# Kernel tuning notes

Measured on AMD Instinct MI355X. Metric: run time of the kernel, lower is better.

The kernel has to match this reference:

```python
import jax, jax.numpy as jnp
import numpy as np

T_STEPS = 64   # number of actions (T-1 in the torch code)
BATCH = 512
STATE = 256
ACTION = 64
BELIEF = 1024
HIDDEN = 1024
EMB = 1024
MIN_STD = 0.1


def setup_inputs() -> dict:
    key = jax.random.key(0)
    ks = jax.random.split(key, 16)
    def w(k, shape):
        return jax.random.normal(k, shape, jnp.float32) * 0.02
    return {
        "s_0": jax.random.normal(ks[0], (BATCH, STATE), jnp.float32),
        "A": jax.random.normal(ks[1], (T_STEPS, BATCH, ACTION), jnp.float32),
        "b_0": jax.random.normal(ks[2], (BATCH, BELIEF), jnp.float32),
        "O": jax.random.normal(ks[3], (T_STEPS, BATCH, EMB), jnp.float32),
        "M": jnp.ones((T_STEPS, BATCH, 1), jnp.float32),
        "noise_pri": jax.random.normal(ks[4], (T_STEPS, BATCH, STATE), jnp.float32),
        "noise_pos": jax.random.normal(ks[5], (T_STEPS, BATCH, STATE), jnp.float32),
        # learned parameters (torch nn.Linear convention: y = x @ W.T + b)
        "W_sa": w(ks[6], (BELIEF, STATE + ACTION)), "b_sa": jnp.zeros((BELIEF,), jnp.float32),
        "W_ih": w(ks[7], (3 * BELIEF, BELIEF)), "b_ih": jnp.zeros((3 * BELIEF,), jnp.float32),
        "W_hh": w(ks[8], (3 * BELIEF, BELIEF)), "b_hh": jnp.zeros((3 * BELIEF,), jnp.float32),
        "W_bpri": w(ks[9], (HIDDEN, BELIEF)), "b_bpri": jnp.zeros((HIDDEN,), jnp.float32),
        "W_spri": w(ks[10], (2 * STATE, HIDDEN)), "b_spri": jnp.zeros((2 * STATE,), jnp.float32),
        "W_bpos": w(ks[11], (HIDDEN, BELIEF + EMB)), "b_bpos": jnp.zeros((HIDDEN,), jnp.float32),
        "W_spos": w(ks[12], (2 * STATE, HIDDEN)), "b_spos": jnp.zeros((2 * STATE,), jnp.float32),
    }


def reference(s_0, A, b_0, O, M, noise_pri, noise_pos,
              W_sa, b_sa, W_ih, b_ih, W_hh, b_hh,
              W_bpri, b_bpri, W_spri, b_spri,
              W_bpos, b_bpos, W_spos, b_spos):
    act = jax.nn.relu  # cfg.activation_function = 'relu'

    def gru_cell(x, h):
        # torch GRUCell gate order: r, z, n
        gi = x @ W_ih.T + b_ih      # [B, 3*BELIEF]
        gh = h @ W_hh.T + b_hh
        i_r, i_z, i_n = jnp.split(gi, 3, axis=1)
        h_r, h_z, h_n = jnp.split(gh, 3, axis=1)
        r = jax.nn.sigmoid(i_r + h_r)
        z = jax.nn.sigmoid(i_z + h_z)
        n = jnp.tanh(i_n + r * h_n)
        return (1.0 - z) * n + z * h

    def step(carry, xs):
        b, s = carry  # belief [B,BELIEF], posterior state [B,STATE]
        a_t, o_t, m_t, eps_p, eps_q = xs
        s_in = s * m_t  # non-terminal mask
        x = act(jnp.concatenate([s_in, a_t], axis=1) @ W_sa.T + b_sa)
        b_new = gru_cell(x, b)
        # prior
        pri = act(b_new @ W_bpri.T + b_bpri) @ W_spri.T + b_spri
        mu_p, hp = jnp.split(pri, 2, axis=1)
        std_p = jax.nn.softplus(hp) + MIN_STD
        s_p = mu_p + std_p * eps_p
        # posterior (uses current observation embedding)
        pos = act(jnp.concatenate([b_new, o_t], axis=1) @ W_bpos.T + b_bpos) @ W_spos.T + b_spos
        mu_q, hq = jnp.split(pos, 2, axis=1)
        std_q = jax.nn.softplus(hq) + MIN_STD
        s_q = mu_q + std_q * eps_q
        return (b_new, s_q), (b_new, s_p, mu_p, std_p, s_q, mu_q, std_q)

    (_, _), ys = jax.lax.scan(step, (b_0, s_0), (A, O, M, noise_pri, noise_pos))
    B_out, S_pri, MU_pri, STD_pri, S_pos, MU_pos, STD_pos = ys
    return B_out, S_pri, MU_pri, STD_pri, S_pos, MU_pos, STD_pos
```

## Files before the change

### kernel.cpp

```cpp
#include <hip/hip_runtime.h>
#include <hip/hip_bf16.h>
#include <math.h>

typedef short bf16x8 __attribute__((ext_vector_type(8)));
typedef float f32x4 __attribute__((ext_vector_type(4)));
typedef unsigned short u16;

#define NT 64
#define NB 512
#define NS 256
#define NA 64
#define NBEL 1024

#define OUT_B      0
#define OUT_SPRI   33554432
#define OUT_MUPRI  41943040
#define OUT_STDPRI 50331648
#define OUT_SPOS   58720256
#define OUT_MUPOS  67108864
#define OUT_STDPOS 75497472

__device__ __forceinline__ f32x4 mfma16(bf16x8 a, bf16x8 b, f32x4 c) {
  return __builtin_amdgcn_mfma_f32_16x16x32_bf16(a, b, c, 0, 0, 0);
}

__device__ __forceinline__ u16 f2bf(float f) {
  union { float f; unsigned u; } v; v.f = f;
  return (u16)((v.u + 0x7FFFu + ((v.u >> 16) & 1u)) >> 16);
}

__device__ __forceinline__ bf16x8 ld8bf(const u16* p) { return *(const bf16x8*)p; }

__device__ __forceinline__ bf16x8 cvt8(const float* p) {
  const float4 lo = *(const float4*)p;
  const float4 hi = *(const float4*)(p + 4);
  bf16x8 v;
  v[0] = (short)f2bf(lo.x); v[1] = (short)f2bf(lo.y);
  v[2] = (short)f2bf(lo.z); v[3] = (short)f2bf(lo.w);
  v[4] = (short)f2bf(hi.x); v[5] = (short)f2bf(hi.y);
  v[6] = (short)f2bf(hi.z); v[7] = (short)f2bf(hi.w);
  return v;
}

__device__ __forceinline__ float sigm(float x) { return 1.f / (1.f + __expf(-x)); }
__device__ __forceinline__ float softplus_(float x) {
  if (x > 20.f) return x;
  return log1pf(__expf(x));
}

#define ZACC(acc) { acc[0][0] = (f32x4){0.f,0.f,0.f,0.f}; acc[0][1] = (f32x4){0.f,0.f,0.f,0.f}; \
                    acc[1][0] = (f32x4){0.f,0.f,0.f,0.f}; acc[1][1] = (f32x4){0.f,0.f,0.f,0.f}; }

#define Q4(acc, a0v, a1v, b0v, b1v) \
  acc[0][0] = mfma16(a0v, b0v, acc[0][0]); \
  acc[0][1] = mfma16(a0v, b1v, acc[0][1]); \
  acc[1][0] = mfma16(a1v, b0v, acc[1][0]); \
  acc[1][1] = mfma16(a1v, b1v, acc[1][1]);

__device__ __forceinline__ void red_write(float* L, f32x4 (&acc)[2][2], int l) {
  const int base = l * 16;
#pragma unroll
  for (int i = 0; i < 2; ++i)
#pragma unroll
    for (int j = 0; j < 2; ++j)
#pragma unroll
      for (int q = 0; q < 4; ++q)
        L[base + (i * 2 + j) * 4 + q] = acc[i][j][q];
}
__device__ __forceinline__ void red_add(const float* L, f32x4 (&acc)[2][2], int l) {
  const int base = l * 16;
#pragma unroll
  for (int i = 0; i < 2; ++i)
#pragma unroll
    for (int j = 0; j < 2; ++j)
#pragma unroll
      for (int q = 0; q < 4; ++q)
        acc[i][j][q] += L[base + (i * 2 + j) * 4 + q];
}

__device__ __forceinline__ void setflag_blk(unsigned* f) {
  __syncthreads();
  if (threadIdx.x == 0)
    __hip_atomic_fetch_add(f, 1u, __ATOMIC_RELEASE, __HIP_MEMORY_SCOPE_AGENT);
}
__device__ __forceinline__ void waitflag_blk(unsigned* f, unsigned target) {
  if (threadIdx.x == 0) {
    while (__hip_atomic_load(f, __ATOMIC_RELAXED, __HIP_MEMORY_SCOPE_AGENT) < target)
      __builtin_amdgcn_s_sleep(2);
    (void)__hip_atomic_load(f, __ATOMIC_ACQUIRE, __HIP_MEMORY_SCOPE_AGENT);
  }
  __syncthreads();
}

__global__ __launch_bounds__(256) void cvt_weights_k(
    const float* __restrict__ wsa, const float* __restrict__ wih,
    const float* __restrict__ whh, const float* __restrict__ wbpri,
    const float* __restrict__ wspri, const float* __restrict__ wbpos,
    const float* __restrict__ wspos, u16* __restrict__ dst) {
  const int S0 = 327680;
  const int S1 = S0 + 3145728;
  const int S2 = S1 + 3145728;
  const int S3 = S2 + 1048576;
  const int S4 = S3 + 524288;
  const int S5 = S4 + 2097152;
  const int S6 = S5 + 524288;
  for (int i = blockIdx.x * blockDim.x + threadIdx.x; i < S6;
       i += gridDim.x * blockDim.x) {
    float v;
    if (i < S0) v = wsa[i];
    else if (i < S1) v = wih[i - S0];
    else if (i < S2) v = whh[i - S1];
    else if (i < S3) v = wbpri[i - S2];
    else if (i < S4) v = wspri[i - S3];
    else if (i < S5) v = wbpos[i - S4];
    else v = wspos[i - S5];
    dst[i] = f2bf(v);
  }
}

__global__ __launch_bounds__(256) void init_carry_k(
    const float* __restrict__ s0, const float* __restrict__ b0,
    const float* __restrict__ Mptr, u16* __restrict__ smask,
    u16* __restrict__ bbf0, float* __restrict__ hf,
    unsigned* __restrict__ flags) {
  for (int i = blockIdx.x * blockDim.x + threadIdx.x; i < NB * NBEL;
       i += gridDim.x * blockDim.x) {
    float b = b0[i];
    bbf0[i] = f2bf(b);
    hf[i] = b;
    if (i < NB * NS) {
      int row = i >> 8;
      smask[i] = f2bf(s0[i] * Mptr[row]);
    }
    if (i < NT) flags[i] = 0;
  }
}

__device__ __forceinline__ void dev_spri(
    int g, int wid, int kh, int r16, int kq, int l, int tt,
    const u16* __restrict__ hpri, const u16* __restrict__ wspri,
    const float* __restrict__ bspri, const float* __restrict__ npri,
    float* __restrict__ out, float* lred0, float* lred1) {
  const int bm = g >> 2, bn = g & 3;
  const int row0 = bm * 64 + (wid >> 1) * 32;
  const int c0 = bn * 64 + (wid & 1) * 32;
  f32x4 am[2][2], ah[2][2];
  ZACC(am); ZACC(ah);
  const u16* A0 = hpri + (row0 + r16) * NBEL + kh * 512 + kq * 8;
  const u16* A1 = A0 + 16 * NBEL;
  const u16* Bm0 = wspri + (size_t)(c0 + r16) * NBEL + kh * 512 + kq * 8;
  const u16* Bm1 = Bm0 + 16 * NBEL;
  const u16* Bh0 = wspri + (size_t)(c0 + 256 + r16) * NBEL + kh * 512 + kq * 8;
  const u16* Bh1 = Bh0 + 16 * NBEL;
#pragma unroll 4
  for (int k = 0; k < 512; k += 32) {
    bf16x8 a0 = ld8bf(A0 + k), a1 = ld8bf(A1 + k);
    bf16x8 m0 = ld8bf(Bm0 + k), m1 = ld8bf(Bm1 + k);
    Q4(am, a0, a1, m0, m1);
    bf16x8 h0 = ld8bf(Bh0 + k), h1 = ld8bf(Bh1 + k);
    Q4(ah, a0, a1, h0, h1);
  }
  if (kh == 1) {
    red_write(lred0, am, l);
    red_write(lred1, ah, l);
  }
  __syncthreads();
  if (kh == 0) {
    red_add(lred0, am, l);
    red_add(lred1, ah, l);
#pragma unroll
    for (int i = 0; i < 2; ++i)
#pragma unroll
      for (int j = 0; j < 2; ++j)
#pragma unroll
        for (int q = 0; q < 4; ++q) {
          const int row = row0 + i * 16 + kq * 4 + q;
          const int c = c0 + j * 16 + r16;
          const size_t idx = (size_t)tt * (NB * NS) + (size_t)row * NS + c;
          const float mu = am[i][j][q] + bspri[c];
          const float hp = ah[i][j][q] + bspri[c + 256];
          const float sd = softplus_(hp) + 0.1f;
          out[OUT_SPRI + idx] = mu + sd * npri[idx];
          out[OUT_MUPRI + idx] = mu;
          out[OUT_STDPRI + idx] = sd;
        }
  }
}

__device__ __forceinline__ void dev_x(
    int g, int wid, int kh, int r16, int kq, int l, int t,
    const u16* __restrict__ smask, const float* __restrict__ Af,
    const u16* __restrict__ wsa, const float* __restrict__ bsa,
    u16* __restrict__ xg, float* lred) {
  const int bm = g >> 4, bn = g & 15;
  const int row0 = bm * 64 + (wid >> 1) * 32;
  const int col0 = bn * 64 + (wid & 1) * 32;
  f32x4 acc[2][2]; ZACC(acc);
  const u16* A0 = smask + (row0 + r16) * NS + kq * 8;
  const u16* A1 = A0 + 16 * NS;
  const u16* B0 = wsa + (size_t)(col0 + r16) * 320 + kq * 8;
  const u16* B1 = B0 + 16 * 320;
  if (kh == 0) {
#pragma unroll
    for (int k = 0; k < 160; k += 32) {
      bf16x8 a0 = ld8bf(A0 + k), a1 = ld8bf(A1 + k);
      bf16x8 b0 = ld8bf(B0 + k), b1 = ld8bf(B1 + k);
      Q4(acc, a0, a1, b0, b1);
    }
  } else {
#pragma unroll
    for (int k = 160; k < 256; k += 32) {
      bf16x8 a0 = ld8bf(A0 + k), a1 = ld8bf(A1 + k);
      bf16x8 b0 = ld8bf(B0 + k), b1 = ld8bf(B1 + k);
      Q4(acc, a0, a1, b0, b1);
    }
    const float* F0 = Af + (size_t)t * (NB * NA) + (size_t)(row0 + r16) * NA + kq * 8;
    const float* F1 = F0 + 16 * NA;
    const u16* C0 = wsa + (size_t)(col0 + r16) * 320 + 256 + kq * 8;
    const u16* C1 = C0 + 16 * 320;
#pragma unroll
    for (int k = 0; k < 64; k += 32) {
      bf16x8 a0 = cvt8(F0 + k), a1 = cvt8(F1 + k);
      bf16x8 b0 = ld8bf(C0 + k), b1 = ld8bf(C1 + k);
      Q4(acc, a0, a1, b0, b1);
    }
    red_write(lred, acc, l);
  }
  __syncthreads();
  if (kh == 0) {
    red_add(lred, acc, l);
#pragma unroll
    for (int i = 0; i < 2; ++i)
#pragma unroll
      for (int j = 0; j < 2; ++j)
#pragma unroll
        for (int q = 0; q < 4; ++q) {
          const int row = row0 + i * 16 + kq * 4 + q;
          const int col = col0 + j * 16 + r16;
          xg[row * NBEL + col] = f2bf(fmaxf(acc[i][j][q] + bsa[col], 0.f));
        }
  }
}

__global__ __launch_bounds__(512, 2) void kX0(
    const u16* __restrict__ smask, const float* __restrict__ Af,
    const u16* __restrict__ wsa, const float* __restrict__ bsa,
    u16* __restrict__ xg, const float* __restrict__ Of,
    const u16* __restrict__ wbpos, float* __restrict__ hbO0) {
  __shared__ float lred[4][1024];
  const int l = threadIdx.x & 63, r16 = l & 15, kq = l >> 4;
  const int wid8 = threadIdx.x >> 6;
  const int wid = wid8 & 3, kh = wid8 >> 2;
  if (blockIdx.x < 128) {
    dev_x(blockIdx.x, wid, kh, r16, kq, l, 0, smask, Af, wsa, bsa, xg,
          lred[wid]);
  } else {
    const int g = blockIdx.x - 128, bm = g >> 4, bn = g & 15;
    const int row0 = bm * 64 + (wid >> 1) * 32;
    const int col0 = bn * 64 + (wid & 1) * 32;
    f32x4 acc[2][2]; ZACC(acc);
    const float* F0 = Of + (row0 + r16) * NBEL + kh * 512 + kq * 8;
    const float* F1 = F0 + 16 * NBEL;
    const u16* B0 = wbpos + (size_t)(col0 + r16) * 2048 + 1024 + kh * 512 + kq * 8;
    const u16* B1 = B0 + 16 * 2048;
#pragma unroll 4
    for (int k = 0; k < 512; k += 32) {
      bf16x8 a0 = cvt8(F0 + k), a1 = cvt8(F1 + k);
      bf16x8 b0 = ld8bf(B0 + k), b1 = ld8bf(B1 + k);
      Q4(acc, a0, a1, b0, b1);
    }
    if (kh == 1) red_write(lred[wid], acc, l);
    __syncthreads();
    if (kh == 0) {
      red_add(lred[wid], acc, l);
#pragma unroll
      for (int i = 0; i < 2; ++i)
#pragma unroll
        for (int j = 0; j < 2; ++j)
#pragma unroll
          for (int q = 0; q < 4; ++q) {
            const int row = row0 + i * 16 + kq * 4 + q;
            const int col = col0 + j * 16 + r16;
            hbO0[row * NBEL + col] = acc[i][j][q];
          }
    }
  }
}

__global__ __launch_bounds__(512, 2) void kL1(
    const u16* __restrict__ xg, const u16* __restrict__ bprev,
    const u16* __restrict__ wih, const u16* __restrict__ whh,
    const float* __restrict__ bih, const float* __restrict__ bhh,
    float* __restrict__ hf, u16* __restrict__ bcur, float* __restrict__ out,
    const u16* __restrict__ hpri, const u16* __restrict__ wspri,
    const float* __restrict__ bspri, const float* __restrict__ npri, int t) {
  __shared__ float lred[4][3][1024];
  const int l = threadIdx.x & 63, r16 = l & 15, kq = l >> 4;
  const int wid8 = threadIdx.x >> 6;
  const int wid = wid8 & 3, kh = wid8 >> 2;
  if (blockIdx.x < 128) {
    const int g = blockIdx.x, bm = g >> 4, bn = g & 15;
    const int row0 = bm * 64 + (wid >> 1) * 32;
    const int col0 = bn * 64 + (wid & 1) * 32;
    f32x4 ar[2][2], az[2][2], an[2][2];
    ZACC(ar); ZACC(az); ZACC(an);
    const u16* Asrc = (kh == 0) ? xg : bprev;
    const u16* W = (kh == 0) ? wih : whh;
    const u16* A0 = Asrc + (row0 + r16) * NBEL + kq * 8;
    const u16* A1 = A0 + 16 * NBEL;
    const u16* Br0 = W + (size_t)(col0 + r16) * NBEL + kq * 8;
    const u16* Br1 = Br0 + 16 * NBEL;
    const u16* Bz0 = W + (size_t)(col0 + 1024 + r16) * NBEL + kq * 8;
    const u16* Bz1 = Bz0 + 16 * NBEL;
    const u16* Bn0 = W + (size_t)(col0 + 2048 + r16) * NBEL + kq * 8;
    const u16* Bn1 = Bn0 + 16 * NBEL;
#pragma unroll 4
    for (int k = 0; k < NBEL; k += 32) {
      bf16x8 a0 = ld8bf(A0 + k), a1 = ld8bf(A1 + k);
      bf16x8 b0 = ld8bf(Br0 + k), b1 = ld8bf(Br1 + k);
      Q4(ar, a0, a1, b0, b1);
      bf16x8 c0 = ld8bf(Bz0 + k), c1 = ld8bf(Bz1 + k);
      Q4(az, a0, a1, c0, c1);
      bf16x8 d0 = ld8bf(Bn0 + k), d1 = ld8bf(Bn1 + k);
      Q4(an, a0, a1, d0, d1);
    }
    if (kh == 1) {
      red_write(&lred[wid][0][0], ar, l);
      red_write(&lred[wid][1][0], az, l);
      red_write(&lred[wid][2][0], an, l);
    }
    __syncthreads();
    if (kh == 0) {
      const int base = l * 16;
#pragma unroll
      for (int i = 0; i < 2; ++i)
#pragma unroll
        for (int j = 0; j < 2; ++j)
#pragma unroll
          for (int q = 0; q < 4; ++q) {
            const int row = row0 + i * 16 + kq * 4 + q;
            const int c = col0 + j * 16 + r16;
            const int li = base + (i * 2 + j) * 4 + q;
            const float r = sigm(ar[i][j][q] + bih[c] + lred[wid][0][li] + bhh[c]);
            const float z = sigm(az[i][j][q] + bih[c + 1024] + lred[wid][1][li] + bhh[c + 1024]);
            const float n = tanhf(an[i][j][q] + bih[c + 2048] +
                                  r * (lred[wid][2][li] + bhh[c + 2048]));
            const float h = hf[row * NBEL + c];
            const float bnew = (1.f - z) * n + z * h;
            hf[row * NBEL + c] = bnew;
            bcur[row * NBEL + c] = f2bf(bnew);
            out[OUT_B + (size_t)t * (NB * NBEL) + row * NBEL + c] = bnew;
          }
    }
  } else if (t >= 1) {
    dev_spri(blockIdx.x - 128, wid, kh, r16, kq, l, t - 1,
             hpri, wspri, bspri, npri, out,
             &lred[wid][0][0], &lred[wid][1][0]);
  }
}

__global__ __launch_bounds__(512, 2) void kL2(
    const u16* __restrict__ bcur, const u16* __restrict__ wbpos,
    const float* __restrict__ bbpos, const float* __restrict__ hbOc,
    u16* __restrict__ hbbf,
    const u16* __restrict__ wbpri, const float* __restrict__ bbpri,
    u16* __restrict__ hpri,
    const float* __restrict__ Of, float* __restrict__ hbOn, int t) {
  __shared__ float lred[4][1024];
  const int l = threadIdx.x & 63, r16 = l & 15, kq = l >> 4;
  const int wid8 = threadIdx.x >> 6;
  const int wid = wid8 & 3, kh = wid8 >> 2;
  if (blockIdx.x < 128) {
    const int g = blockIdx.x, bm = g >> 4, bn = g & 15;
    const int row0 = bm * 64 + (wid >> 1) * 32;
    const int col0 = bn * 64 + (wid & 1) * 32;
    f32x4 acc[2][2]; ZACC(acc);
    const u16* A0 = bcur + (row0 + r16) * NBEL + kh * 512 + kq * 8;
    const u16* A1 = A0 + 16 * NBEL;
    const u16* B0 = wbpos + (size_t)(col0 + r16) * 2048 + kh * 512 + kq * 8;
    const u16* B1 = B0 + 16 * 2048;
#pragma unroll 4
    for (int k = 0; k < 512; k += 32) {
      bf16x8 a0 = ld8bf(A0 + k), a1 = ld8bf(A1 + k);
      bf16x8 b0 = ld8bf(B0 + k), b1 = ld8bf(B1 + k);
      Q4(acc, a0, a1, b0, b1);
    }
    if (kh == 1) red_write(lred[wid], acc, l);
    __syncthreads();
    if (kh == 0) {
      red_add(lred[wid], acc, l);
#pragma unroll
      for (int i = 0; i < 2; ++i)
#pragma unroll
        for (int j = 0; j < 2; ++j)
#pragma unroll
          for (int q = 0; q < 4; ++q) {
            const int row = row0 + i * 16 + kq * 4 + q;
            const int col = col0 + j * 16 + r16;
            const float v = acc[i][j][q] + hbOc[row * NBEL + col] + bbpos[col];
            hbbf[row * NBEL + col] = f2bf(fmaxf(v, 0.f));
          }
    }
  } else if (blockIdx.x < 256) {
    const int g = blockIdx.x - 128, bm = g >> 4, bn = g & 15;
    const int row0 = bm * 64 + (wid >> 1) * 32;
    const int col0 = bn * 64 + (wid & 1) * 32;
    f32x4 acc[2][2]; ZACC(acc);
    const u16* A0 = bcur + (row0 + r16) * NBEL + kh * 512 + kq * 8;
    const u16* A1 = A0 + 16 * NBEL;
    const u16* B0 = wbpri + (size_t)(col0 + r16) * NBEL + kh * 512 + kq * 8;
    const u16* B1 = B0 + 16 * NBEL;
#pragma unroll 4
    for (int k = 0; k < 512; k += 32) {
      bf16x8 a0 = ld8bf(A0 + k), a1 = ld8bf(A1 + k);
      bf16x8 b0 = ld8bf(B0 + k), b1 = ld8bf(B1 + k);
      Q4(acc, a0, a1, b0, b1);
    }
    if (kh == 1) red_write(lred[wid], acc, l);
    __syncthreads();
    if (kh == 0) {
      red_add(lred[wid], acc, l);
#pragma unroll
      for (int i = 0; i < 2; ++i)
#pragma unroll
        for (int j = 0; j < 2; ++j)
#pragma unroll
          for (int q = 0; q < 4; ++q) {
            const int row = row0 + i * 16 + kq * 4 + q;
            const int col = col0 + j * 16 + r16;
            hpri[row * NBEL + col] = f2bf(fmaxf(acc[i][j][q] + bbpri[col], 0.f));
          }
    }
  } else {
    if (t + 1 >= NT) return;
    const int g = blockIdx.x - 256, bm = g >> 4, bn = g & 15;
    const int row0 = bm * 64 + (wid >> 1) * 32;
    const int col0 = bn * 64 + (wid & 1) * 32;
    f32x4 acc[2][2]; ZACC(acc);
    const float* F0 = Of + (size_t)(t + 1) * (NB * NBEL) + (row0 + r16) * NBEL + kh * 512 + kq * 8;
    const float* F1 = F0 + 16 * NBEL;
    const u16* B0 = wbpos + (size_t)(col0 + r16) * 2048 + 1024 + kh * 512 + kq * 8;
    const u16* B1 = B0 + 16 * 2048;
#pragma unroll 4
    for (int k = 0; k < 512; k += 32) {
      bf16x8 a0 = cvt8(F0 + k), a1 = cvt8(F1 + k);
      bf16x8 b0 = ld8bf(B0 + k), b1 = ld8bf(B1 + k);
      Q4(acc, a0, a1, b0, b1);
    }
    if (kh == 1) red_write(lred[wid], acc, l);
    __syncthreads();
    if (kh == 0) {
      red_add(lred[wid], acc, l);
#pragma unroll
      for (int i = 0; i < 2; ++i)
#pragma unroll
        for (int j = 0; j < 2; ++j)
#pragma unroll
          for (int q = 0; q < 4; ++q) {
            const int row = row0 + i * 16 + kq * 4 + q;
            const int col = col0 + j * 16 + r16;
            hbOn[row * NBEL + col] = acc[i][j][q];
          }
    }
  }
}

__global__ __launch_bounds__(512, 2) void kLX(
    const u16* __restrict__ hbbf, const u16* __restrict__ wspos,
    const float* __restrict__ bspos, const float* __restrict__ npos,
    const float* __restrict__ Mptr, float* __restrict__ out,
    u16* __restrict__ smask,
    const float* __restrict__ Af, const u16* __restrict__ wsa,
    const float* __restrict__ bsa, u16* __restrict__ xg,
    const u16* __restrict__ hpri, const u16* __restrict__ wspri,
    const float* __restrict__ bspri, const float* __restrict__ npri,
    unsigned* __restrict__ flags, int t) {
  __shared__ float lred[4][2][1024];
  const int l = threadIdx.x & 63, r16 = l & 15, kq = l >> 4;
  const int wid8 = threadIdx.x >> 6;
  const int wid = wid8 & 3, kh = wid8 >> 2;
  if (blockIdx.x < 32) {
    const int g = blockIdx.x, bm = g >> 2, bn = g & 3;
    const int row0 = bm * 64 + (wid >> 1) * 32;
    const int c0 = bn * 64 + (wid & 1) * 32;
    f32x4 am[2][2], ah[2][2];
    ZACC(am); ZACC(ah);
    const u16* A0 = hbbf + (row0 + r16) * NBEL + kh * 512 + kq * 8;
    const u16* A1 = A0 + 16 * NBEL;
    const u16* Bm0 = wspos + (size_t)(c0 + r16) * NBEL + kh * 512 + kq * 8;
    const u16* Bm1 = Bm0 + 16 * NBEL;
    const u16* Bh0 = wspos + (size_t)(c0 + 256 + r16) * NBEL + kh * 512 + kq * 8;
    const u16* Bh1 = Bh0 + 16 * NBEL;
#pragma unroll 4
    for (int k = 0; k < 512; k += 32) {
      bf16x8 a0 = ld8bf(A0 + k), a1 = ld8bf(A1 + k);
      bf16x8 m0 = ld8bf(Bm0 + k), m1 = ld8bf(Bm1 + k);
      Q4(am, a0, a1, m0, m1);
      bf16x8 h0 = ld8bf(Bh0 + k), h1 = ld8bf(Bh1 + k);
      Q4(ah, a0, a1, h0, h1);
    }
    if (kh == 1) {
      red_write(&lred[wid][0][0], am, l);
      red_write(&lred[wid][1][0], ah, l);
    }
    __syncthreads();
    if (kh == 0) {
      red_add(&lred[wid][0][0], am, l);
      red_add(&lred[wid][1][0], ah, l);
#pragma unroll
      for (int i = 0; i < 2; ++i)
#pragma unroll
        for (int j = 0; j < 2; ++j)
#pragma unroll
          for (int q = 0; q < 4; ++q) {
            const int row = row0 + i * 16 + kq * 4 + q;
            const int c = c0 + j * 16 + r16;
            const float mu = am[i][j][q] + bspos[c];
            const float hq = ah[i][j][q] + bspos[c + 256];
            const float sd = softplus_(hq) + 0.1f;
            const size_t idx = (size_t)t * (NB * NS) + (size_t)row * NS + c;
            const float sq = mu + sd * npos[idx];
            out[OUT_SPOS + idx] = sq;
            out[OUT_MUPOS + idx] = mu;
            out[OUT_STDPOS + idx] = sd;
            const float mn = (t < NT - 1) ? Mptr[(t + 1) * NB + row] : 1.f;
            smask[row * NS + c] = f2bf(sq * mn);
          }
    }
    setflag_blk(&flags[t]);
  } else if (blockIdx.x < 160) {
    if (t + 1 >= NT) return;
    waitflag_blk(&flags[t], 32);
    dev_x(blockIdx.x - 32, wid, kh, r16, kq, l, t + 1, smask, Af, wsa, bsa,
          xg, &lred[wid][0][0]);
  } else {
    if (t == NT - 1)
      dev_spri(blockIdx.x - 160, wid, kh, r16, kq, l, t,
               hpri, wspri, bspri, npri, out,
               &lred[wid][0][0], &lred[wid][1][0]);
  }
}

extern "C" void kernel_launch(void* const* d_in, const int* in_sizes, int n_in,
                              void* d_out, int out_size, void* d_ws, size_t ws_size,
                              hipStream_t stream) {
  const float* s0 = (const float*)d_in[0];
  const float* Af = (const float*)d_in[1];
  const float* b0 = (const float*)d_in[2];
  const float* Of = (const float*)d_in[3];
  const float* Mp = (const float*)d_in[4];
  const float* npri = (const float*)d_in[5];
  const float* npos = (const float*)d_in[6];
  const float* Wsa = (const float*)d_in[7];
  const float* bsa = (const float*)d_in[8];
  const float* Wih = (const float*)d_in[9];
  const float* bih = (const float*)d_in[10];
  const float* Whh = (const float*)d_in[11];
  const float* bhh = (const float*)d_in[12];
  const float* Wbpri = (const float*)d_in[13];
  const float* bbpri = (const float*)d_in[14];
  const float* Wspri = (const float*)d_in[15];
  const float* bspri = (const float*)d_in[16];
  const float* Wbpos = (const float*)d_in[17];
  const float* bbpos = (const float*)d_in[18];
  const float* Wspos = (const float*)d_in[19];
  const float* bspos = (const float*)d_in[20];

  float* out = (float*)d_out;
  char* ws = (char*)d_ws;
  u16* wbase   = (u16*)ws;
  u16* wsa_b   = wbase;
  u16* wih_b   = wbase + 327680;
  u16* whh_b   = wbase + 3473408;
  u16* wbpri_b = wbase + 6619136;
  u16* wspri_b = wbase + 7667712;
  u16* wbpos_b = wbase + 8192000;
  u16* wspos_b = wbase + 10289152;
  u16*   smask = (u16*)  (ws + 21626880);
  u16*   bbf0  = (u16*)  (ws + 21889024);
  u16*   bbf1  = (u16*)  (ws + 22937600);
  float* hf    = (float*)(ws + 23986176);
  u16*   xg    = (u16*)  (ws + 26083328);
  float* hbO0  = (float*)(ws + 27131904);
  float* hbO1  = (float*)(ws + 29229056);
  u16*   hbbf  = (u16*)  (ws + 31326208);
  u16*   hpri  = (u16*)  (ws + 32374784);
  unsigned* flags = (unsigned*)(ws + 33423360);

  cvt_weights_k<<<2048, 256, 0, stream>>>(Wsa, Wih, Whh, Wbpri, Wspri, Wbpos,
                                          Wspos, wbase);
  init_carry_k<<<2048, 256, 0, stream>>>(s0, b0, Mp, smask, bbf0, hf, flags);
  kX0<<<256, 512, 0, stream>>>(smask, Af, wsa_b, bsa, xg, Of, wbpos_b, hbO0);

  for (int t = 0; t < NT; ++t) {
    const u16* bprev = (t & 1) ? bbf1 : bbf0;
    u16* bcur = (t & 1) ? bbf0 : bbf1;
    float* hbOc = (t & 1) ? hbO1 : hbO0;
    float* hbOn = (t & 1) ? hbO0 : hbO1;
    kL1<<<160, 512, 0, stream>>>(xg, bprev, wih_b, whh_b, bih, bhh, hf, bcur,
                                 out, hpri, wspri_b, bspri, npri, t);
    kL2<<<384, 512, 0, stream>>>(bcur, wbpos_b, bbpos, hbOc, hbbf,
                                 wbpri_b, bbpri, hpri, Of, hbOn, t);
    kLX<<<192, 512, 0, stream>>>(hbbf, wspos_b, bspos, npos, Mp, out, smask,
                                 Af, wsa_b, bsa, xg,
                                 hpri, wspri_b, bspri, npri, flags, t);
  }
}
```

Baseline: 9.406 ms.

## Hoist hidden-state GRU GEMM off critical path and merge per-step kernels

The b@W_hh GEMM for the next step is now computed early in the mid-step kernel, stored as bf16 gh buffers, and consumed by the GRU kernel, which then only does the x@W_ih GEMM. The old kL2 and kLX launches are merged into one kernel that uses three flag arrays to order the posterior, next-x and prior-state sections inside the grid. Several GEMM tiles also drop the intra-block K-split reduction in favour of full-K 128-wide tiles. This shortens the serial chain and removes one launch per step, at the cost of bf16 rounding of the gh values, extra workspace, and a risk of spin-wait deadlock if blocks that wait on flags are resident before the blocks that set them.

```diff
diff --git a/kernel.cpp b/kernel.cpp
--- a/kernel.cpp
+++ b/kernel.cpp
@@ -27,6 +27,9 @@
 __device__ __forceinline__ u16 f2bf(float f) {
   union { float f; unsigned u; } v; v.f = f;
   return (u16)((v.u + 0x7FFFu + ((v.u >> 16) & 1u)) >> 16);
+}
+__device__ __forceinline__ float bf2f(u16 h) {
+  union { unsigned u; float f; } v; v.u = ((unsigned)h) << 16; return v.f;
 }
 
 __device__ __forceinline__ bf16x8 ld8bf(const u16* p) { return *(const bf16x8*)p; }
@@ -56,6 +59,35 @@
   acc[0][1] = mfma16(a0v, b1v, acc[0][1]); \
   acc[1][0] = mfma16(a1v, b0v, acc[1][0]); \
   acc[1][1] = mfma16(a1v, b1v, acc[1][1]);
+
+__device__ __forceinline__ void gtile(f32x4 (&acc)[2][2],
+    const u16* __restrict__ A, int lda, const u16* __restrict__ B, int ldb,
+    int K, int r16, int kq) {
+  const u16* A0 = A + r16 * lda + kq * 8;
+  const u16* A1 = A0 + 16 * lda;
+  const u16* B0 = B + (size_t)r16 * ldb + kq * 8;
+  const u16* B1 = B0 + 16 * ldb;
+#pragma unroll 4
+  for (int k = 0; k < K; k += 32) {
+    bf16x8 a0 = ld8bf(A0 + k), a1 = ld8bf(A1 + k);
+    bf16x8 b0 = ld8bf(B0 + k), b1 = ld8bf(B1 + k);
+    Q4(acc, a0, a1, b0, b1);
+  }
+}
+__device__ __forceinline__ void gtileF(f32x4 (&acc)[2][2],
+    const float* __restrict__ A, int lda, const u16* __restrict__ B, int ldb,
+    int K, int r16, int kq) {
+  const float* A0 = A + r16 * lda + kq * 8;
+  const float* A1 = A0 + 16 * lda;
+  const u16* B0 = B + (size_t)r16 * ldb + kq * 8;
+  const u16* B1 = B0 + 16 * ldb;
+#pragma unroll 2
+  for (int k = 0; k < K; k += 32) {
+    bf16x8 a0 = cvt8(A0 + k), a1 = cvt8(A1 + k);
+    bf16x8 b0 = ld8bf(B0 + k), b1 = ld8bf(B1 + k);
+    Q4(acc, a0, a1, b0, b1);
+  }
+}
 
 __device__ __forceinline__ void red_write(float* L, f32x4 (&acc)[2][2], int l) {
   const int base = l * 16;
@@ -121,20 +153,21 @@
 __global__ __launch_bounds__(256) void init_carry_k(
     const float* __restrict__ s0, const float* __restrict__ b0,
     const float* __restrict__ Mptr, u16* __restrict__ smask,
-    u16* __restrict__ bbf0, float* __restrict__ hf,
+    u16* __restrict__ bbf, float* __restrict__ hf,
     unsigned* __restrict__ flags) {
   for (int i = blockIdx.x * blockDim.x + threadIdx.x; i < NB * NBEL;
        i += gridDim.x * blockDim.x) {
     float b = b0[i];
-    bbf0[i] = f2bf(b);
+    bbf[i] = f2bf(b);
     hf[i] = b;
     if (i < NB * NS) {
       int row = i >> 8;
       smask[i] = f2bf(s0[i] * Mptr[row]);
     }
-    if (i < NT) flags[i] = 0;
-  }
-}
+    if (i < 3 * NT) flags[i] = 0;
+  }
+}
+
 
 __device__ __forceinline__ void dev_spri(
     int g, int wid, int kh, int r16, int kq, int l, int tt,
@@ -187,48 +220,62 @@
   }
 }
 
-__device__ __forceinline__ void dev_x(
-    int g, int wid, int kh, int r16, int kq, int l, int t,
+__device__ __forceinline__ void dev_x64(
+    int g, int wid8, int r16, int kq, int t,
     const u16* __restrict__ smask, const float* __restrict__ Af,
     const u16* __restrict__ wsa, const float* __restrict__ bsa,
-    u16* __restrict__ xg, float* lred) {
-  const int bm = g >> 4, bn = g & 15;
-  const int row0 = bm * 64 + (wid >> 1) * 32;
-  const int col0 = bn * 64 + (wid & 1) * 32;
+    u16* __restrict__ xg) {
+  const int row0 = (g >> 3) * 64 + (wid8 >> 2) * 32;
+  const int col0 = (g & 7) * 128 + (wid8 & 3) * 32;
   f32x4 acc[2][2]; ZACC(acc);
-  const u16* A0 = smask + (row0 + r16) * NS + kq * 8;
-  const u16* A1 = A0 + 16 * NS;
-  const u16* B0 = wsa + (size_t)(col0 + r16) * 320 + kq * 8;
-  const u16* B1 = B0 + 16 * 320;
-  if (kh == 0) {
-#pragma unroll
-    for (int k = 0; k < 160; k += 32) {
-      bf16x8 a0 = ld8bf(A0 + k), a1 = ld8bf(A1 + k);
-      bf16x8 b0 = ld8bf(B0 + k), b1 = ld8bf(B1 + k);
-      Q4(acc, a0, a1, b0, b1);
-    }
-  } else {
-#pragma unroll
-    for (int k = 160; k < 256; k += 32) {
-      bf16x8 a0 = ld8bf(A0 + k), a1 = ld8bf(A1 + k);
-      bf16x8 b0 = ld8bf(B0 + k), b1 = ld8bf(B1 + k);
-      Q4(acc, a0, a1, b0, b1);
-    }
-    const float* F0 = Af + (size_t)t * (NB * NA) + (size_t)(row0 + r16) * NA + kq * 8;
-    const float* F1 = F0 + 16 * NA;
-    const u16* C0 = wsa + (size_t)(col0 + r16) * 320 + 256 + kq * 8;
-    const u16* C1 = C0 + 16 * 320;
-#pragma unroll
-    for (int k = 0; k < 64; k += 32) {
-      bf16x8 a0 = cvt8(F0 + k), a1 = cvt8(F1 + k);
-      bf16x8 b0 = ld8bf(C0 + k), b1 = ld8bf(C1 + k);
-      Q4(acc, a0, a1, b0, b1);
-    }
-    red_write(lred, acc, l);
-  }
-  __syncthreads();
-  if (kh == 0) {
-    red_add(lred, acc, l);
+  gtile(acc, smask + row0 * NS, NS, wsa + (size_t)col0 * 320, 320, 256, r16, kq);
+  gtileF(acc, Af + (size_t)t * (NB * NA) + (size_t)row0 * NA, NA,
+         wsa + (size_t)col0 * 320 + 256, 320, 64, r16, kq);
+#pragma unroll
+  for (int i = 0; i < 2; ++i)
+#pragma unroll
+    for (int j = 0; j < 2; ++j)
+#pragma unroll
+      for (int q = 0; q < 4; ++q) {
+        const int row = row0 + i * 16 + kq * 4 + q;
+        const int col = col0 + j * 16 + r16;
+        xg[row * NBEL + col] = f2bf(fmaxf(acc[i][j][q] + bsa[col], 0.f));
+      }
+}
+
+__device__ __forceinline__ void dev_hbO64(
+    int g, int wid8, int r16, int kq,
+    const float* __restrict__ OfT, const u16* __restrict__ wbpos,
+    float* __restrict__ hbOn) {
+  const int row0 = (g >> 3) * 64 + (wid8 >> 2) * 32;
+  const int col0 = (g & 7) * 128 + (wid8 & 3) * 32;
+  f32x4 acc[2][2]; ZACC(acc);
+  gtileF(acc, OfT + (size_t)row0 * NBEL, NBEL,
+         wbpos + (size_t)col0 * 2048 + 1024, 2048, 1024, r16, kq);
+#pragma unroll
+  for (int i = 0; i < 2; ++i)
+#pragma unroll
+    for (int j = 0; j < 2; ++j)
+#pragma unroll
+      for (int q = 0; q < 4; ++q) {
+        const int row = row0 + i * 16 + kq * 4 + q;
+        const int col = col0 + j * 16 + r16;
+        hbOn[row * NBEL + col] = acc[i][j][q];
+      }
+}
+
+__device__ __forceinline__ void dev_gh96(
+    int g, int wid8, int r16, int kq,
+    const u16* __restrict__ bsrc, const u16* __restrict__ whh,
+    const float* __restrict__ bhh, u16* __restrict__ ghn) {
+  const int bm = g / 12, bc = g % 12;
+  const int row0 = bm * 64 + (wid8 >> 2) * 32;
+#pragma unroll
+  for (int jt = 0; jt < 2; ++jt) {
+    const int col0 = bc * 256 + (wid8 & 3) * 32 + jt * 128;
+    f32x4 acc[2][2]; ZACC(acc);
+    gtile(acc, bsrc + row0 * NBEL, NBEL, whh + (size_t)col0 * NBEL, NBEL,
+          1024, r16, kq);
 #pragma unroll
     for (int i = 0; i < 2; ++i)
 #pragma unroll
@@ -237,60 +284,53 @@
         for (int q = 0; q < 4; ++q) {
           const int row = row0 + i * 16 + kq * 4 + q;
           const int col = col0 + j * 16 + r16;
-          xg[row * NBEL + col] = f2bf(fmaxf(acc[i][j][q] + bsa[col], 0.f));
+          ghn[row * 3072 + col] = f2bf(acc[i][j][q] + bhh[col]);
         }
   }
+}
+
+__device__ __forceinline__ void dev_bpri64(
+    int g, int wid8, int r16, int kq,
+    const u16* __restrict__ bcur, const u16* __restrict__ wbpri,
+    const float* __restrict__ bbpri, u16* __restrict__ hpri) {
+  const int row0 = (g >> 3) * 64 + (wid8 >> 2) * 32;
+  const int col0 = (g & 7) * 128 + (wid8 & 3) * 32;
+  f32x4 acc[2][2]; ZACC(acc);
+  gtile(acc, bcur + row0 * NBEL, NBEL, wbpri + (size_t)col0 * NBEL, NBEL,
+        1024, r16, kq);
+#pragma unroll
+  for (int i = 0; i < 2; ++i)
+#pragma unroll
+    for (int j = 0; j < 2; ++j)
+#pragma unroll
+      for (int q = 0; q < 4; ++q) {
+        const int row = row0 + i * 16 + kq * 4 + q;
+        const int col = col0 + j * 16 + r16;
+        hpri[row * NBEL + col] = f2bf(fmaxf(acc[i][j][q] + bbpri[col], 0.f));
+      }
 }
 
 __global__ __launch_bounds__(512, 2) void kX0(
     const u16* __restrict__ smask, const float* __restrict__ Af,
     const u16* __restrict__ wsa, const float* __restrict__ bsa,
     u16* __restrict__ xg, const float* __restrict__ Of,
-    const u16* __restrict__ wbpos, float* __restrict__ hbO0) {
-  __shared__ float lred[4][1024];
+    const u16* __restrict__ wbpos, float* __restrict__ hbO0,
+    const u16* __restrict__ bbf, const u16* __restrict__ whh,
+    const float* __restrict__ bhh, u16* __restrict__ ghA) {
   const int l = threadIdx.x & 63, r16 = l & 15, kq = l >> 4;
   const int wid8 = threadIdx.x >> 6;
-  const int wid = wid8 & 3, kh = wid8 >> 2;
-  if (blockIdx.x < 128) {
-    dev_x(blockIdx.x, wid, kh, r16, kq, l, 0, smask, Af, wsa, bsa, xg,
-          lred[wid]);
+  if (blockIdx.x < 64) {
+    dev_x64(blockIdx.x, wid8, r16, kq, 0, smask, Af, wsa, bsa, xg);
+  } else if (blockIdx.x < 128) {
+    dev_hbO64(blockIdx.x - 64, wid8, r16, kq, Of, wbpos, hbO0);
   } else {
-    const int g = blockIdx.x - 128, bm = g >> 4, bn = g & 15;
-    const int row0 = bm * 64 + (wid >> 1) * 32;
-    const int col0 = bn * 64 + (wid & 1) * 32;
-    f32x4 acc[2][2]; ZACC(acc);
-    const float* F0 = Of + (row0 + r16) * NBEL + kh * 512 + kq * 8;
-    const float* F1 = F0 + 16 * NBEL;
-    const u16* B0 = wbpos + (size_t)(col0 + r16) * 2048 + 1024 + kh * 512 + kq * 8;
-    const u16* B1 = B0 + 16 * 2048;
-#pragma unroll 4
-    for (int k = 0; k < 512; k += 32) {
-      bf16x8 a0 = cvt8(F0 + k), a1 = cvt8(F1 + k);
-      bf16x8 b0 = ld8bf(B0 + k), b1 = ld8bf(B1 + k);
-      Q4(acc, a0, a1, b0, b1);
-    }
-    if (kh == 1) red_write(lred[wid], acc, l);
-    __syncthreads();
-    if (kh == 0) {
-      red_add(lred[wid], acc, l);
-#pragma unroll
-      for (int i = 0; i < 2; ++i)
-#pragma unroll
-        for (int j = 0; j < 2; ++j)
-#pragma unroll
-          for (int q = 0; q < 4; ++q) {
-            const int row = row0 + i * 16 + kq * 4 + q;
-            const int col = col0 + j * 16 + r16;
-            hbO0[row * NBEL + col] = acc[i][j][q];
-          }
-    }
-  }
-}
-
-__global__ __launch_bounds__(512, 2) void kL1(
-    const u16* __restrict__ xg, const u16* __restrict__ bprev,
-    const u16* __restrict__ wih, const u16* __restrict__ whh,
-    const float* __restrict__ bih, const float* __restrict__ bhh,
+    dev_gh96(blockIdx.x - 128, wid8, r16, kq, bbf, whh, bhh, ghA);
+  }
+}
+
+__global__ __launch_bounds__(512, 2) void kG(
+    const u16* __restrict__ xg, const u16* __restrict__ wih,
+    const float* __restrict__ bih, const u16* __restrict__ ghc,
     float* __restrict__ hf, u16* __restrict__ bcur, float* __restrict__ out,
     const u16* __restrict__ hpri, const u16* __restrict__ wspri,
     const float* __restrict__ bspri, const float* __restrict__ npri, int t) {
@@ -304,18 +344,16 @@
     const int col0 = bn * 64 + (wid & 1) * 32;
     f32x4 ar[2][2], az[2][2], an[2][2];
     ZACC(ar); ZACC(az); ZACC(an);
-    const u16* Asrc = (kh == 0) ? xg : bprev;
-    const u16* W = (kh == 0) ? wih : whh;
-    const u16* A0 = Asrc + (row0 + r16) * NBEL + kq * 8;
+    const u16* A0 = xg + (row0 + r16) * NBEL + kh * 512 + kq * 8;
     const u16* A1 = A0 + 16 * NBEL;
-    const u16* Br0 = W + (size_t)(col0 + r16) * NBEL + kq * 8;
+    const u16* Br0 = wih + (size_t)(col0 + r16) * NBEL + kh * 512 + kq * 8;
     const u16* Br1 = Br0 + 16 * NBEL;
-    const u16* Bz0 = W + (size_t)(col0 + 1024 + r16) * NBEL + kq * 8;
+    const u16* Bz0 = wih + (size_t)(col0 + 1024 + r16) * NBEL + kh * 512 + kq * 8;
     const u16* Bz1 = Bz0 + 16 * NBEL;
-    const u16* Bn0 = W + (size_t)(col0 + 2048 + r16) * NBEL + kq * 8;
+    const u16* Bn0 = wih + (size_t)(col0 + 2048 + r16) * NBEL + kh * 512 + kq * 8;
     const u16* Bn1 = Bn0 + 16 * NBEL;
 #pragma unroll 4
-    for (int k = 0; k < NBEL; k += 32) {
+    for (int k = 0; k < 512; k += 32) {
       bf16x8 a0 = ld8bf(A0 + k), a1 = ld8bf(A1 + k);
       bf16x8 b0 = ld8bf(Br0 + k), b1 = ld8bf(Br1 + k);
       Q4(ar, a0, a1, b0, b1);
@@ -341,10 +379,13 @@
             const int row = row0 + i * 16 + kq * 4 + q;
             const int c = col0 + j * 16 + r16;
             const int li = base + (i * 2 + j) * 4 + q;
-            const float r = sigm(ar[i][j][q] + bih[c] + lred[wid][0][li] + bhh[c]);
-            const float z = sigm(az[i][j][q] + bih[c + 1024] + lred[wid][1][li] + bhh[c + 1024]);
-            const float n = tanhf(an[i][j][q] + bih[c + 2048] +
-                                  r * (lred[wid][2][li] + bhh[c + 2048]));
+            const u16* ghrow = ghc + row * 3072;
+            const float r = sigm(ar[i][j][q] + lred[wid][0][li] + bih[c] +
+                                 bf2f(ghrow[c]));
+            const float z = sigm(az[i][j][q] + lred[wid][1][li] + bih[c + 1024] +
+                                 bf2f(ghrow[c + 1024]));
+            const float n = tanhf(an[i][j][q] + lred[wid][2][li] + bih[c + 2048] +
+                                  r * bf2f(ghrow[c + 2048]));
             const float h = hf[row * NBEL + c];
             const float bnew = (1.f - z) * n + z * h;
             hf[row * NBEL + c] = bnew;
@@ -359,14 +400,26 @@
   }
 }
 
-__global__ __launch_bounds__(512, 2) void kL2(
+__global__ __launch_bounds__(512, 2) void kM(
     const u16* __restrict__ bcur, const u16* __restrict__ wbpos,
     const float* __restrict__ bbpos, const float* __restrict__ hbOc,
     u16* __restrict__ hbbf,
     const u16* __restrict__ wbpri, const float* __restrict__ bbpri,
     u16* __restrict__ hpri,
-    const float* __restrict__ Of, float* __restrict__ hbOn, int t) {
-  __shared__ float lred[4][1024];
+    const u16* __restrict__ whh, const float* __restrict__ bhh,
+    u16* __restrict__ ghn,
+    const float* __restrict__ Of, float* __restrict__ hbOn,
+    const u16* __restrict__ wspos, const float* __restrict__ bspos,
+    const float* __restrict__ npos, const float* __restrict__ Mptr,
+    u16* __restrict__ smask,
+    const float* __restrict__ Af, const u16* __restrict__ wsa,
+    const float* __restrict__ bsa, u16* __restrict__ xg,
+    const u16* __restrict__ wspri, const float* __restrict__ bspri,
+    const float* __restrict__ npri,
+    float* __restrict__ out,
+    unsigned* __restrict__ fH, unsigned* __restrict__ fS,
+    unsigned* __restrict__ fB, int t) {
+  __shared__ float lred[4][2][1024];
   const int l = threadIdx.x & 63, r16 = l & 15, kq = l >> 4;
   const int wid8 = threadIdx.x >> 6;
   const int wid = wid8 & 3, kh = wid8 >> 2;
@@ -385,10 +438,10 @@
       bf16x8 b0 = ld8bf(B0 + k), b1 = ld8bf(B1 + k);
       Q4(acc, a0, a1, b0, b1);
     }
-    if (kh == 1) red_write(lred[wid], acc, l);
+    if (kh == 1) red_write(&lred[wid][0][0], acc, l);
     __syncthreads();
     if (kh == 0) {
-      red_add(lred[wid], acc, l);
+      red_add(&lred[wid][0][0], acc, l);
 #pragma unroll
       for (int i = 0; i < 2; ++i)
 #pragma unroll
@@ -401,86 +454,20 @@
             hbbf[row * NBEL + col] = f2bf(fmaxf(v, 0.f));
           }
     }
-  } else if (blockIdx.x < 256) {
-    const int g = blockIdx.x - 128, bm = g >> 4, bn = g & 15;
-    const int row0 = bm * 64 + (wid >> 1) * 32;
-    const int col0 = bn * 64 + (wid & 1) * 32;
-    f32x4 acc[2][2]; ZACC(acc);
-    const u16* A0 = bcur + (row0 + r16) * NBEL + kh * 512 + kq * 8;
-    const u16* A1 = A0 + 16 * NBEL;
-    const u16* B0 = wbpri + (size_t)(col0 + r16) * NBEL + kh * 512 + kq * 8;
-    const u16* B1 = B0 + 16 * NBEL;
-#pragma unroll 4
-    for (int k = 0; k < 512; k += 32) {
-      bf16x8 a0 = ld8bf(A0 + k), a1 = ld8bf(A1 + k);
-      bf16x8 b0 = ld8bf(B0 + k), b1 = ld8bf(B1 + k);
-      Q4(acc, a0, a1, b0, b1);
-    }
-    if (kh == 1) red_write(lred[wid], acc, l);
-    __syncthreads();
-    if (kh == 0) {
-      red_add(lred[wid], acc, l);
-#pragma unroll
-      for (int i = 0; i < 2; ++i)
-#pragma unroll
-        for (int j = 0; j < 2; ++j)
-#pragma unroll
-          for (int q = 0; q < 4; ++q) {
-            const int row = row0 + i * 16 + kq * 4 + q;
-            const int col = col0 + j * 16 + r16;
-            hpri[row * NBEL + col] = f2bf(fmaxf(acc[i][j][q] + bbpri[col], 0.f));
-          }
-    }
-  } else {
+    setflag_blk(&fH[t]);
+  } else if (blockIdx.x < 192) {
+    dev_bpri64(blockIdx.x - 128, wid8, r16, kq, bcur, wbpri, bbpri, hpri);
+    setflag_blk(&fB[t]);
+  } else if (blockIdx.x < 288) {
     if (t + 1 >= NT) return;
-    const int g = blockIdx.x - 256, bm = g >> 4, bn = g & 15;
-    const int row0 = bm * 64 + (wid >> 1) * 32;
-    const int col0 = bn * 64 + (wid & 1) * 32;
-    f32x4 acc[2][2]; ZACC(acc);
-    const float* F0 = Of + (size_t)(t + 1) * (NB * NBEL) + (row0 + r16) * NBEL + kh * 512 + kq * 8;
-    const float* F1 = F0 + 16 * NBEL;
-    const u16* B0 = wbpos + (size_t)(col0 + r16) * 2048 + 1024 + kh * 512 + kq * 8;
-    const u16* B1 = B0 + 16 * 2048;
-#pragma unroll 4
-    for (int k = 0; k < 512; k += 32) {
-      bf16x8 a0 = cvt8(F0 + k), a1 = cvt8(F1 + k);
-      bf16x8 b0 = ld8bf(B0 + k), b1 = ld8bf(B1 + k);
-      Q4(acc, a0, a1, b0, b1);
-    }
-    if (kh == 1) red_write(lred[wid], acc, l);
-    __syncthreads();
-    if (kh == 0) {
-      red_add(lred[wid], acc, l);
-#pragma unroll
-      for (int i = 0; i < 2; ++i)
-#pragma unroll
-        for (int j = 0; j < 2; ++j)
-#pragma unroll
-          for (int q = 0; q < 4; ++q) {
-            const int row = row0 + i * 16 + kq * 4 + q;
-            const int col = col0 + j * 16 + r16;
-            hbOn[row * NBEL + col] = acc[i][j][q];
-          }
-    }
-  }
-}
-
-__global__ __launch_bounds__(512, 2) void kLX(
-    const u16* __restrict__ hbbf, const u16* __restrict__ wspos,
-    const float* __restrict__ bspos, const float* __restrict__ npos,
-    const float* __restrict__ Mptr, float* __restrict__ out,
-    u16* __restrict__ smask,
-    const float* __restrict__ Af, const u16* __restrict__ wsa,
-    const float* __restrict__ bsa, u16* __restrict__ xg,
-    const u16* __restrict__ hpri, const u16* __restrict__ wspri,
-    const float* __restrict__ bspri, const float* __restrict__ npri,
-    unsigned* __restrict__ flags, int t) {
-  __shared__ float lred[4][2][1024];
-  const int l = threadIdx.x & 63, r16 = l & 15, kq = l >> 4;
-  const int wid8 = threadIdx.x >> 6;
-  const int wid = wid8 & 3, kh = wid8 >> 2;
-  if (blockIdx.x < 32) {
-    const int g = blockIdx.x, bm = g >> 2, bn = g & 3;
+    dev_gh96(blockIdx.x - 192, wid8, r16, kq, bcur, whh, bhh, ghn);
+  } else if (blockIdx.x < 352) {
+    if (t + 1 >= NT) return;
+    dev_hbO64(blockIdx.x - 288, wid8, r16, kq,
+              Of + (size_t)(t + 1) * (NB * NBEL), wbpos, hbOn);
+  } else if (blockIdx.x < 384) {
+    waitflag_blk(&fH[t], 128);
+    const int g = blockIdx.x - 352, bm = g >> 2, bn = g & 3;
     const int row0 = bm * 64 + (wid >> 1) * 32;
     const int c0 = bn * 64 + (wid & 1) * 32;
     f32x4 am[2][2], ah[2][2];
@@ -527,17 +514,17 @@
             smask[row * NS + c] = f2bf(sq * mn);
           }
     }
-    setflag_blk(&flags[t]);
-  } else if (blockIdx.x < 160) {
+    setflag_blk(&fS[t]);
+  } else if (blockIdx.x < 448) {
     if (t + 1 >= NT) return;
-    waitflag_blk(&flags[t], 32);
-    dev_x(blockIdx.x - 32, wid, kh, r16, kq, l, t + 1, smask, Af, wsa, bsa,
-          xg, &lred[wid][0][0]);
+    waitflag_blk(&fS[t], 32);
+    dev_x64(blockIdx.x - 384, wid8, r16, kq, t + 1, smask, Af, wsa, bsa, xg);
   } else {
-    if (t == NT - 1)
-      dev_spri(blockIdx.x - 160, wid, kh, r16, kq, l, t,
-               hpri, wspri, bspri, npri, out,
-               &lred[wid][0][0], &lred[wid][1][0]);
+    if (t != NT - 1) return;
+    waitflag_blk(&fB[t], 64);
+    dev_spri(blockIdx.x - 448, wid, kh, r16, kq, l, t,
+             hpri, wspri, bspri, npri, out,
+             &lred[wid][0][0], &lred[wid][1][0]);
   }
 }
 
@@ -577,32 +564,38 @@
   u16* wbpos_b = wbase + 8192000;
   u16* wspos_b = wbase + 10289152;
   u16*   smask = (u16*)  (ws + 21626880);
-  u16*   bbf0  = (u16*)  (ws + 21889024);
-  u16*   bbf1  = (u16*)  (ws + 22937600);
-  float* hf    = (float*)(ws + 23986176);
-  u16*   xg    = (u16*)  (ws + 26083328);
-  float* hbO0  = (float*)(ws + 27131904);
-  float* hbO1  = (float*)(ws + 29229056);
-  u16*   hbbf  = (u16*)  (ws + 31326208);
-  u16*   hpri  = (u16*)  (ws + 32374784);
-  unsigned* flags = (unsigned*)(ws + 33423360);
+  u16*   bbf   = (u16*)  (ws + 21889024);
+  float* hf    = (float*)(ws + 22937600);
+  u16*   xg    = (u16*)  (ws + 25034752);
+  float* hbO0  = (float*)(ws + 26083328);
+  float* hbO1  = (float*)(ws + 28180480);
+  u16*   hbbf  = (u16*)  (ws + 30277632);
+  u16*   hpri  = (u16*)  (ws + 31326208);
+  u16*   ghA   = (u16*)  (ws + 32374784);
+  u16*   ghB   = (u16*)  (ws + 35520512);
+  unsigned* flags = (unsigned*)(ws + 38666240);
+  unsigned* fH = flags, *fS = flags + NT, *fB = flags + 2 * NT;
 
   cvt_weights_k<<<2048, 256, 0, stream>>>(Wsa, Wih, Whh, Wbpri, Wspri, Wbpos,
                                           Wspos, wbase);
-  init_carry_k<<<2048, 256, 0, stream>>>(s0, b0, Mp, smask, bbf0, hf, flags);
-  kX0<<<256, 512, 0, stream>>>(smask, Af, wsa_b, bsa, xg, Of, wbpos_b, hbO0);
+  init_carry_k<<<2048, 256, 0, stream>>>(s0, b0, Mp, smask, bbf, hf, flags);
+  kX0<<<224, 512, 0, stream>>>(smask, Af, wsa_b, bsa, xg, Of, wbpos_b, hbO0,
+                               bbf, whh_b, bhh, ghA);
 
   for (int t = 0; t < NT; ++t) {
-    const u16* bprev = (t & 1) ? bbf1 : bbf0;
-    u16* bcur = (t & 1) ? bbf0 : bbf1;
     float* hbOc = (t & 1) ? hbO1 : hbO0;
     float* hbOn = (t & 1) ? hbO0 : hbO1;
-    kL1<<<160, 512, 0, stream>>>(xg, bprev, wih_b, whh_b, bih, bhh, hf, bcur,
-                                 out, hpri, wspri_b, bspri, npri, t);
-    kL2<<<384, 512, 0, stream>>>(bcur, wbpos_b, bbpos, hbOc, hbbf,
-                                 wbpri_b, bbpri, hpri, Of, hbOn, t);
-    kLX<<<192, 512, 0, stream>>>(hbbf, wspos_b, bspos, npos, Mp, out, smask,
-                                 Af, wsa_b, bsa, xg,
-                                 hpri, wspri_b, bspri, npri, flags, t);
-  }
-}
+    u16* ghc = (t & 1) ? ghB : ghA;
+    u16* ghn = (t & 1) ? ghA : ghB;
+    kG<<<160, 512, 0, stream>>>(xg, wih_b, bih, ghc, hf, bbf, out,
+                                hpri, wspri_b, bspri, npri, t);
+    kM<<<480, 512, 0, stream>>>(bbf, wbpos_b, bbpos, hbOc, hbbf,
+                                wbpri_b, bbpri, hpri,
+                                whh_b, bhh, ghn,
+                                Of, hbOn,
+                                wspos_b, bspos, npos, Mp, smask,
+                                Af, wsa_b, bsa, xg,
+                                wspri_b, bspri, npri,
+                                out, fH, fS, fB, t);
+  }
+}
```

Measured after the change: 8.208 ms. 1.15x faster.
